# Kernel optimization log

Hardware: AMD Instinct MI355X
Metric: run time of the kernel (lower is better)

The kernel has to match this reference:

```python
import jax, jax.numpy as jnp
import numpy as np
from jax.scipy.special import logsumexp

DEN_SCALE = 1.0  # den_scale from LFMMILoss.__init__


def _log_marginal(em, seqlens, logA, log_start, log_final):
    """Forward (alpha) recursion of a WFSA in log space.
    em: [B,T,S] per-state emission log-likelihoods; logA: [S,S] or [B,S,S].
    Returns per-sequence log-marginal [B].
    """
    B, T, S = em.shape
    alpha0 = log_start + em[:, 0]  # [B,S]

    def step(alpha, xs):
        em_t, t = xs
        # [B,S,1] + [.,S,S] -> logsumexp over source state
        new = logsumexp(alpha[:, :, None] + logA, axis=1) + em_t
        alpha = jnp.where((t < seqlens)[:, None], new, alpha)
        return alpha, None

    em_t_first = jnp.swapaxes(em, 0, 1)  # [T,B,S]
    alpha, _ = jax.lax.scan(step, alpha0, (em_t_first[1:], jnp.arange(1, T)))
    return logsumexp(alpha + log_final, axis=1)  # [B]


def _fsm_logprob(x, seqlens, logA, log_start, log_final, pdf_ids):
    B, T, _ = x.shape
    if pdf_ids.ndim == 1:  # shared graph (denominator)
        em = x[:, :, pdf_ids]  # [B,T,S]
    else:  # per-utterance graphs (numerators), pdf_ids: [B,S]
        S = pdf_ids.shape[-1]
        idx = jnp.broadcast_to(pdf_ids[:, None, :], (B, T, S))
        em = jnp.take_along_axis(x, idx, axis=2)
    return _log_marginal(em, seqlens, logA, log_start, log_final)


def setup_inputs() -> dict:
    key = jax.random.key(0)
    ks = jax.random.split(key, 10)
    B, T, C = 16, 500, 2048
    S_num, S_den = 64, 512
    inp = jax.random.normal(ks[0], (B, T, C), jnp.float32)
    seqlengths = jax.random.randint(ks[1], (B,), T // 2, T + 1, jnp.int32)
    num_logA = jax.nn.log_softmax(jax.random.normal(ks[2], (B, S_num, S_num), jnp.float32), axis=-1)
    num_log_start = jax.nn.log_softmax(jax.random.normal(ks[3], (B, S_num), jnp.float32), axis=-1)
    num_log_final = jax.nn.log_softmax(jax.random.normal(ks[4], (B, S_num), jnp.float32), axis=-1)
    num_pdf_ids = jax.random.randint(ks[5], (B, S_num), 0, C, jnp.int32)
    den_logA = jax.nn.log_softmax(jax.random.normal(ks[6], (S_den, S_den), jnp.float32), axis=-1)
    den_log_start = jax.nn.log_softmax(jax.random.normal(ks[7], (S_den,), jnp.float32), axis=-1)
    den_log_final = jax.nn.log_softmax(jax.random.normal(ks[8], (S_den,), jnp.float32), axis=-1)
    den_pdf_ids = jax.random.randint(ks[9], (S_den,), 0, C, jnp.int32)
    return {
        "input": inp, "seqlengths": seqlengths,
        "num_logA": num_logA, "num_log_start": num_log_start,
        "num_log_final": num_log_final, "num_pdf_ids": num_pdf_ids,
        "den_logA": den_logA, "den_log_start": den_log_start,
        "den_log_final": den_log_final, "den_pdf_ids": den_pdf_ids,
    }


def reference(input, seqlengths, num_logA, num_log_start, num_log_final,
              num_pdf_ids, den_logA, den_log_start, den_log_final, den_pdf_ids):
    x = jnp.clip(input, -30.0, 30.0)
    num_llh = _fsm_logprob(x, seqlengths, num_logA, num_log_start, num_log_final, num_pdf_ids).sum()
    den_llh = _fsm_logprob(x, seqlengths, den_logA, den_log_start, den_log_final, den_pdf_ids).sum()
    return -(num_llh - DEN_SCALE * den_llh)
```

## Files before the change

kernel.cpp:

```cpp
#include <hip/hip_runtime.h>
#include <math.h>

#define BB 16
#define TT 500
#define CC 2048
#define SN 64
#define SD 512
#define NGRP 16
#define NCB 8
#define NDEN 128
#define NTHR 512
#define SHIFTC 30.0f

#define WSF_DACC   32768
#define WSF_DSCALE 32784
#define WSF_NACC   32800
#define WSF_NSCALE 32816

#define AL(p) __hip_atomic_load((p), __ATOMIC_RELAXED, __HIP_MEMORY_SCOPE_AGENT)
#define AS(p, v) __hip_atomic_store((p), (v), __ATOMIC_RELAXED, __HIP_MEMORY_SCOPE_AGENT)

typedef float f4 __attribute__((ext_vector_type(4)));

__device__ __forceinline__ float wave_max(float v) {
  #pragma unroll
  for (int off = 32; off > 0; off >>= 1) v = fmaxf(v, __shfl_xor(v, off, 64));
  return v;
}
__device__ __forceinline__ float wave_sum(float v) {
  #pragma unroll
  for (int off = 32; off > 0; off >>= 1) v += __shfl_xor(v, off, 64);
  return v;
}
__device__ __forceinline__ unsigned long long pk(unsigned tag, float v) {
  return ((unsigned long long)tag << 32) | (unsigned long long)__float_as_uint(v);
}
__device__ __forceinline__ float clamp30(float v) {
  return fminf(fmaxf(v, -30.f), 30.f);
}
__device__ __forceinline__ float rlane(float v, int k) {
  return __uint_as_float(__builtin_amdgcn_readlane(__float_as_uint(v), k));
}

__device__ __forceinline__ void barrier_lds_only() {
  asm volatile("s_waitcnt lgkmcnt(0)" ::: "memory");
  __builtin_amdgcn_s_barrier();
  asm volatile("" ::: "memory");
}

__global__ __launch_bounds__(NTHR, 1) void fsm_fwd(
    const float* __restrict__ x, const int* __restrict__ seqlens,
    const float* __restrict__ nA, const float* __restrict__ nls,
    const float* __restrict__ nlf, const int* __restrict__ npdf,
    const float* __restrict__ dA, const float* __restrict__ dls,
    const float* __restrict__ dlf, const int* __restrict__ dpdf,
    unsigned long long* __restrict__ p64, float* __restrict__ wsf)
{
  __shared__ float prt[2][8 * 64];
  __shared__ float pmx[2][8];
  const int tid = threadIdx.x;
  const int lane = tid & 63, wv = tid >> 6;

  if (blockIdx.x < NDEN) {
    const int g  = blockIdx.x & 15;
    const int cb = blockIdx.x >> 4;
    const int j0 = cb * 64;

    f4 Areg[16];
    {
      const float* Ap = dA + (wv * 64) * SD + j0 + lane;
      #pragma unroll
      for (int k = 0; k < 64; ++k)
        Areg[k >> 2][k & 3] = __expf(Ap[k * SD]);
      #pragma unroll
      for (int r = 0; r < 16; ++r)
        asm volatile("" : "+v"(Areg[r]));
    }

    unsigned long long* gb0 = p64 + (size_t)g * SD;
    unsigned long long* gb1 = p64 + (size_t)(NGRP + g) * SD;

    int pdfj = 0, sl = 0; float lfj = 0.f, pcur = 0.f, scale = SHIFTC;
    float xc = 0.f;
    if (wv == 0) {
      pdfj = dpdf[j0 + lane];
      lfj  = dlf[j0 + lane];
      sl   = seqlens[g];
      float xv = clamp30(x[g * (TT * CC) + pdfj]);
      pcur = __expf(dls[j0 + lane] + xv - SHIFTC);
      AS(gb0 + j0 + lane, pk(0u, pcur));
      xc = clamp30(x[g * (TT * CC) + CC + pdfj]);
    }

    for (int t = 1; t < TT; ++t) {
      unsigned long long* gin  = (t & 1) ? gb0 : gb1;
      unsigned long long* gout = (t & 1) ? gb1 : gb0;

      const unsigned tg = (unsigned)(t - 1);
      unsigned long long* pa = gin + wv * 64 + lane;
      unsigned long long w;
      for (;;) {
        w = AL(pa);
        if ((unsigned)(w >> 32) == tg) break;
        __builtin_amdgcn_s_sleep(1);
      }
      float pv = __uint_as_float((unsigned)w);

      float cm = wave_max(pv);
      if (lane == 0) pmx[t & 1][wv] = cm;

      float q = 0.f;
      #pragma unroll
      for (int k = 0; k < 64; ++k) {
        float pk_ = rlane(pv, k);
        q = fmaf(pk_, Areg[k >> 2][k & 3], q);
      }
      prt[t & 1][wv * 64 + lane] = q;

      barrier_lds_only();

      if (wv == 0) {
        const float* pb = prt[t & 1];
        float qq = 0.f;
        #pragma unroll
        for (int w8 = 0; w8 < 8; ++w8) qq += pb[w8 * 64 + lane];
        float m = pmx[t & 1][0];
        #pragma unroll
        for (int w8 = 1; w8 < 8; ++w8) m = fmaxf(m, pmx[t & 1][w8]);
        float lm = __logf(m);
        if (t < sl) {
          pcur = qq * __expf(xc - SHIFTC - lm);
          scale += SHIFTC + lm;
        }
        AS(gout + j0 + lane, pk((unsigned)t, pcur));
        if (t + 1 < TT)
          xc = clamp30(x[g * (TT * CC) + (t + 1) * CC + pdfj]);
      }
    }
    if (wv == 0) {
      float part = wave_sum(pcur * __expf(lfj));
      if (lane == 0) {
        atomicAdd(wsf + WSF_DACC + g, part);
        if (cb == 0) wsf[WSF_DSCALE + g] = scale;
      }
    }
  } else {
    const int b = blockIdx.x - NDEN;
    if (wv != 0) return;

    f4 Areg[16];
    {
      const float* Ap = nA + b * SN * SN + lane;
      #pragma unroll
      for (int i = 0; i < 64; ++i)
        Areg[i >> 2][i & 3] = __expf(Ap[i * SN]);
      #pragma unroll
      for (int r = 0; r < 16; ++r)
        asm volatile("" : "+v"(Areg[r]));
    }
    const int   pdfj = npdf[b * SN + lane];
    const float lfj  = nlf[b * SN + lane];
    const int   sl   = seqlens[b];
    float xv0 = clamp30(x[b * (TT * CC) + pdfj]);
    float pcur = __expf(nls[b * SN + lane] + xv0 - SHIFTC);
    float scale = SHIFTC;
    float xn = clamp30(x[b * (TT * CC) + CC + pdfj]);

    for (int t = 1; t < TT; ++t) {
      float xv = xn;
      if (t + 1 < TT)
        xn = clamp30(x[b * (TT * CC) + (t + 1) * CC + pdfj]);
      float pold = pcur;
      float q = 0.f;
      #pragma unroll
      for (int i = 0; i < 64; ++i) {
        float pi = rlane(pold, i);
        q = fmaf(pi, Areg[i >> 2][i & 3], q);
      }
      float lm = __logf(wave_max(pold));
      if (t < sl) {
        pcur = q * __expf(xv - SHIFTC - lm);
        scale += SHIFTC + lm;
      }
    }
    float part = wave_sum(pcur * __expf(lfj));
    if (lane == 0) {
      wsf[WSF_NACC + b]   = part;
      wsf[WSF_NSCALE + b] = scale;
    }
  }
}

__global__ void fsm_final(const float* __restrict__ wsf, float* __restrict__ out) {
  const int tid = threadIdx.x;
  float v = 0.f;
  if (tid < 16)
    v = -(wsf[WSF_NSCALE + tid] + __logf(wsf[WSF_NACC + tid]));
  else if (tid < 32)
    v = (wsf[WSF_DSCALE + tid - 16] + __logf(wsf[WSF_DACC + tid - 16]));
  v = wave_sum(v);
  if (tid == 0) out[0] = v;
}

extern "C" void kernel_launch(void* const* d_in, const int* in_sizes, int n_in,
                              void* d_out, int out_size, void* d_ws, size_t ws_size,
                              hipStream_t stream) {
  const float* x    = (const float*)d_in[0];
  const int*   sql  = (const int*)d_in[1];
  const float* nA   = (const float*)d_in[2];
  const float* nls  = (const float*)d_in[3];
  const float* nlf  = (const float*)d_in[4];
  const int*   npdf = (const int*)d_in[5];
  const float* dA   = (const float*)d_in[6];
  const float* dls  = (const float*)d_in[7];
  const float* dlf  = (const float*)d_in[8];
  const int*   dpdf = (const int*)d_in[9];
  float* out = (float*)d_out;
  unsigned long long* p64 = (unsigned long long*)d_ws;
  float* wsf = (float*)d_ws;
  (void)in_sizes; (void)n_in; (void)out_size; (void)ws_size;

  hipMemsetAsync((char*)d_ws + 131072, 0, 256, stream);
  fsm_fwd<<<NDEN + BB, NTHR, 0, stream>>>(x, sql, nA, nls, nlf, npdf,
                                          dA, dls, dlf, dpdf, p64, wsf);
  fsm_final<<<1, 64, 0, stream>>>(wsf, out);
}
```

Baseline: 878.1 us.

## Interleave four denominator sequences per block to hide cross-block sync latency

Each denominator block now advances four batch sequences round-robin instead of one, so it can work on other sequences while the cross-block exchange for one sequence is still in flight. The grid drops from 128 to 32 active denominator blocks, with 32 more launched and exited immediately. The next sequence's state and emission value are prefetched before the barrier. The output update is spread across all eight waves, eight lanes each, instead of only wave 0. The cost is more serial work per block, one LDS barrier per sequence step, and fewer CUs in use.

```diff
diff --git a/kernel.cpp b/kernel.cpp
--- a/kernel.cpp
+++ b/kernel.cpp
@@ -7,8 +7,9 @@
 #define SN 64
 #define SD 512
 #define NGRP 16
-#define NCB 8
-#define NDEN 128
+#define NSETS 4
+#define GPW 4
+#define NDENSLOT 64
 #define NTHR 512
 #define SHIFTC 30.0f
 
@@ -40,6 +41,10 @@
 }
 __device__ __forceinline__ float rlane(float v, int k) {
   return __uint_as_float(__builtin_amdgcn_readlane(__float_as_uint(v), k));
+}
+__device__ __forceinline__ unsigned long long* recbase(
+    unsigned long long* p64, int g, int tag) {
+  return p64 + ((tag & 1) ? (size_t)(NGRP + g) : (size_t)g) * SD;
 }
 
 __device__ __forceinline__ void barrier_lds_only() {
@@ -56,15 +61,17 @@
     const float* __restrict__ dlf, const int* __restrict__ dpdf,
     unsigned long long* __restrict__ p64, float* __restrict__ wsf)
 {
-  __shared__ float prt[2][8 * 64];
+  __shared__ float prt[2][8][64];
   __shared__ float pmx[2][8];
   const int tid = threadIdx.x;
   const int lane = tid & 63, wv = tid >> 6;
 
-  if (blockIdx.x < NDEN) {
-    const int g  = blockIdx.x & 15;
-    const int cb = blockIdx.x >> 4;
+  if (blockIdx.x < NDENSLOT) {
+    if ((blockIdx.x & 7) >= NSETS) return;
+    const int st = blockIdx.x & 7;
+    const int cb = blockIdx.x >> 3;
     const int j0 = cb * 64;
+    const int gbase = st * GPW;
 
     f4 Areg[16];
     {
@@ -77,75 +84,99 @@
         asm volatile("" : "+v"(Areg[r]));
     }
 
-    unsigned long long* gb0 = p64 + (size_t)g * SD;
-    unsigned long long* gb1 = p64 + (size_t)(NGRP + g) * SD;
-
-    int pdfj = 0, sl = 0; float lfj = 0.f, pcur = 0.f, scale = SHIFTC;
-    float xc = 0.f;
-    if (wv == 0) {
-      pdfj = dpdf[j0 + lane];
-      lfj  = dlf[j0 + lane];
-      sl   = seqlens[g];
-      float xv = clamp30(x[g * (TT * CC) + pdfj]);
-      pcur = __expf(dls[j0 + lane] + xv - SHIFTC);
-      AS(gb0 + j0 + lane, pk(0u, pcur));
-      xc = clamp30(x[g * (TT * CC) + CC + pdfj]);
-    }
+    const int oc   = j0 + 8 * wv + (lane & 7);
+    const int pdfo = dpdf[oc];
+    const float lfo = dlf[oc];
+    const float lso = dls[oc];
+
+    int   sl4[GPW];
+    float pc[GPW], sc[GPW];
+    #pragma unroll
+    for (int gk = 0; gk < GPW; ++gk) {
+      const int g = gbase + gk;
+      sl4[gk] = seqlens[g];
+      sc[gk]  = SHIFTC;
+      pc[gk]  = 0.f;
+      if (lane < 8) {
+        float xv = clamp30(x[(size_t)g * (TT * CC) + pdfo]);
+        pc[gk] = __expf(lso + xv - SHIFTC);
+        AS(recbase(p64, g, 0) + oc, pk(0u, pc[gk]));
+      }
+    }
+    unsigned long long pf = AL(recbase(p64, gbase, 0) + wv * 64 + lane);
+    float xn = 0.f;
+    if (lane < 8)
+      xn = clamp30(x[(size_t)gbase * (TT * CC) + CC + pdfo]);
 
     for (int t = 1; t < TT; ++t) {
-      unsigned long long* gin  = (t & 1) ? gb0 : gb1;
-      unsigned long long* gout = (t & 1) ? gb1 : gb0;
-
-      const unsigned tg = (unsigned)(t - 1);
-      unsigned long long* pa = gin + wv * 64 + lane;
-      unsigned long long w;
-      for (;;) {
-        w = AL(pa);
-        if ((unsigned)(w >> 32) == tg) break;
-        __builtin_amdgcn_s_sleep(1);
-      }
-      float pv = __uint_as_float((unsigned)w);
-
-      float cm = wave_max(pv);
-      if (lane == 0) pmx[t & 1][wv] = cm;
-
-      float q = 0.f;
-      #pragma unroll
-      for (int k = 0; k < 64; ++k) {
-        float pk_ = rlane(pv, k);
-        q = fmaf(pk_, Areg[k >> 2][k & 3], q);
-      }
-      prt[t & 1][wv * 64 + lane] = q;
-
-      barrier_lds_only();
-
-      if (wv == 0) {
-        const float* pb = prt[t & 1];
-        float qq = 0.f;
+      #pragma unroll
+      for (int gk = 0; gk < GPW; ++gk) {
+        const int g   = gbase + gk;
+        const int par = gk & 1;
+        const unsigned tg = (unsigned)(t - 1);
+        unsigned long long* pa = recbase(p64, g, t - 1) + wv * 64 + lane;
+
+        unsigned long long w = pf;
+        while ((unsigned)(w >> 32) != tg) {
+          w = AL(pa);
+          if ((unsigned)(w >> 32) == tg) break;
+          __builtin_amdgcn_s_sleep(1);
+        }
+        float pv = __uint_as_float((unsigned)w);
+
+        float cm = wave_max(pv);
+        if (lane == 0) pmx[par][wv] = cm;
+
+        float q = 0.f;
         #pragma unroll
-        for (int w8 = 0; w8 < 8; ++w8) qq += pb[w8 * 64 + lane];
-        float m = pmx[t & 1][0];
-        #pragma unroll
-        for (int w8 = 1; w8 < 8; ++w8) m = fmaxf(m, pmx[t & 1][w8]);
-        float lm = __logf(m);
-        if (t < sl) {
-          pcur = qq * __expf(xc - SHIFTC - lm);
-          scale += SHIFTC + lm;
+        for (int k = 0; k < 64; ++k)
+          q = fmaf(rlane(pv, k), Areg[k >> 2][k & 3], q);
+        prt[par][wv][lane] = q;
+
+        const int  gn = (gk == GPW - 1) ? gbase : g + 1;
+        const int  tn = (gk == GPW - 1) ? t + 1 : t;
+        const bool hn = (tn < TT);
+        float xq = xn;
+        if (hn) {
+          pf = AL(recbase(p64, gn, tn - 1) + wv * 64 + lane);
+          if (lane < 8)
+            xn = clamp30(x[(size_t)gn * (TT * CC) + (size_t)tn * CC + pdfo]);
         }
-        AS(gout + j0 + lane, pk((unsigned)t, pcur));
-        if (t + 1 < TT)
-          xc = clamp30(x[g * (TT * CC) + (t + 1) * CC + pdfj]);
-      }
-    }
-    if (wv == 0) {
-      float part = wave_sum(pcur * __expf(lfj));
-      if (lane == 0) {
+
+        barrier_lds_only();
+
+        if (lane < 8) {
+          float m = pmx[par][0];
+          #pragma unroll
+          for (int w8 = 1; w8 < 8; ++w8) m = fmaxf(m, pmx[par][w8]);
+          float lm = __logf(m);
+          float qq = 0.f;
+          #pragma unroll
+          for (int w8 = 0; w8 < 8; ++w8) qq += prt[par][w8][8 * wv + lane];
+          if (t < sl4[gk]) {
+            pc[gk] = qq * __expf(xq - SHIFTC - lm);
+            sc[gk] += SHIFTC + lm;
+          }
+          AS(recbase(p64, g, t) + oc, pk((unsigned)t, pc[gk]));
+        }
+      }
+    }
+
+    #pragma unroll
+    for (int gk = 0; gk < GPW; ++gk) {
+      const int g = gbase + gk;
+      float v = (lane < 8) ? pc[gk] * __expf(lfo) : 0.f;
+      float part = wave_sum(v);
+      if (lane == 0)
         atomicAdd(wsf + WSF_DACC + g, part);
-        if (cb == 0) wsf[WSF_DSCALE + g] = scale;
-      }
+    }
+    if (cb == 0 && wv == 0 && lane == 0) {
+      #pragma unroll
+      for (int gk = 0; gk < GPW; ++gk)
+        wsf[WSF_DSCALE + gbase + gk] = sc[gk];
     }
   } else {
-    const int b = blockIdx.x - NDEN;
+    const int b = blockIdx.x - NDENSLOT;
     if (wv != 0) return;
 
     f4 Areg[16];
@@ -161,15 +192,15 @@
     const int   pdfj = npdf[b * SN + lane];
     const float lfj  = nlf[b * SN + lane];
     const int   sl   = seqlens[b];
-    float xv0 = clamp30(x[b * (TT * CC) + pdfj]);
+    float xv0 = clamp30(x[(size_t)b * (TT * CC) + pdfj]);
     float pcur = __expf(nls[b * SN + lane] + xv0 - SHIFTC);
     float scale = SHIFTC;
-    float xn = clamp30(x[b * (TT * CC) + CC + pdfj]);
+    float xnn = clamp30(x[(size_t)b * (TT * CC) + CC + pdfj]);
 
     for (int t = 1; t < TT; ++t) {
-      float xv = xn;
+      float xv = xnn;
       if (t + 1 < TT)
-        xn = clamp30(x[b * (TT * CC) + (t + 1) * CC + pdfj]);
+        xnn = clamp30(x[(size_t)b * (TT * CC) + (size_t)(t + 1) * CC + pdfj]);
       float pold = pcur;
       float q = 0.f;
       #pragma unroll
@@ -221,7 +252,7 @@
   (void)in_sizes; (void)n_in; (void)out_size; (void)ws_size;
 
   hipMemsetAsync((char*)d_ws + 131072, 0, 256, stream);
-  fsm_fwd<<<NDEN + BB, NTHR, 0, stream>>>(x, sql, nA, nls, nlf, npdf,
-                                          dA, dls, dlf, dpdf, p64, wsf);
+  fsm_fwd<<<NDENSLOT + BB, NTHR, 0, stream>>>(x, sql, nA, nls, nlf, npdf,
+                                              dA, dls, dlf, dpdf, p64, wsf);
   fsm_final<<<1, 64, 0, stream>>>(wsf, out);
 }
```

New measurement: 2.922 ms. +232.8%, slower.

## Poll cross-block partials with sc0 loads, fall back to atomics, prefetch emissions earlier

Applied to the files above, without the earlier changes.

Cross-block polling of the denominator alpha buffer now first uses sc0-qualified global loads under a small retry budget. If polling keeps failing it falls back to agent-scope atomic loads and eventually disables the fast path. Each producer store is duplicated as an sc0 store plus an atomic store. Emission loads are issued earlier, before the LDS reduction in the denominator path and two steps ahead in the numerator path, to hide global latency. The aim is lower inter-block communication latency per timestep. The cost is extra stores and a reliance on cache-coherence behaviour of sc0 on this hardware.

```diff
diff --git a/kernel.cpp b/kernel.cpp
--- a/kernel.cpp
+++ b/kernel.cpp
@@ -11,6 +11,7 @@
 #define NDEN 128
 #define NTHR 512
 #define SHIFTC 30.0f
+#define SC0_BUDGET 8
 
 #define WSF_DACC   32768
 #define WSF_DSCALE 32784
@@ -21,6 +22,18 @@
 #define AS(p, v) __hip_atomic_store((p), (v), __ATOMIC_RELAXED, __HIP_MEMORY_SCOPE_AGENT)
 
 typedef float f4 __attribute__((ext_vector_type(4)));
+
+__device__ __forceinline__ unsigned long long ld_sc0(const unsigned long long* p) {
+  unsigned long long r;
+  asm volatile("global_load_dwordx2 %0, %1, off sc0\n\t"
+               "s_waitcnt vmcnt(0)"
+               : "=v"(r) : "v"((unsigned long long)p) : "memory");
+  return r;
+}
+__device__ __forceinline__ void st_sc0(unsigned long long* p, unsigned long long v) {
+  asm volatile("global_store_dwordx2 %0, %1, off sc0"
+               :: "v"((unsigned long long)p), "v"(v) : "memory");
+}
 
 __device__ __forceinline__ float wave_max(float v) {
   #pragma unroll
@@ -81,16 +94,21 @@
     unsigned long long* gb1 = p64 + (size_t)(NGRP + g) * SD;
 
     int pdfj = 0, sl = 0; float lfj = 0.f, pcur = 0.f, scale = SHIFTC;
-    float xc = 0.f;
+    float xraw = 0.f;
     if (wv == 0) {
       pdfj = dpdf[j0 + lane];
       lfj  = dlf[j0 + lane];
       sl   = seqlens[g];
       float xv = clamp30(x[g * (TT * CC) + pdfj]);
       pcur = __expf(dls[j0 + lane] + xv - SHIFTC);
-      AS(gb0 + j0 + lane, pk(0u, pcur));
-      xc = clamp30(x[g * (TT * CC) + CC + pdfj]);
-    }
+      unsigned long long rec = pk(0u, pcur);
+      unsigned long long* gp = gb0 + j0 + lane;
+      st_sc0(gp, rec);
+      AS(gp, rec);
+      xraw = x[g * (TT * CC) + CC + pdfj];
+    }
+
+    int budget = SC0_BUDGET, streak = 0;
 
     for (int t = 1; t < TT; ++t) {
       unsigned long long* gin  = (t & 1) ? gb0 : gb1;
@@ -98,13 +116,27 @@
 
       const unsigned tg = (unsigned)(t - 1);
       unsigned long long* pa = gin + wv * 64 + lane;
-      unsigned long long w;
-      for (;;) {
-        w = AL(pa);
-        if ((unsigned)(w >> 32) == tg) break;
+      unsigned long long w = 0;
+      bool ok = false;
+      for (int s = 0; s < budget; ++s) {
+        w = ld_sc0(pa);
+        if ((unsigned)(w >> 32) == tg) { ok = true; break; }
         __builtin_amdgcn_s_sleep(1);
       }
+      const bool allok = __all((int)ok);
+      if (!ok) {
+        for (;;) {
+          w = AL(pa);
+          if ((unsigned)(w >> 32) == tg) break;
+          __builtin_amdgcn_s_sleep(1);
+        }
+      }
+      if (budget) { if (!allok) { if (++streak >= 4) budget = 0; } else streak = 0; }
       float pv = __uint_as_float((unsigned)w);
+
+      float xnew = 0.f;
+      if (wv == 0 && t + 1 < TT)
+        xnew = x[g * (TT * CC) + (t + 1) * CC + pdfj];
 
       float cm = wave_max(pv);
       if (lane == 0) pmx[t & 1][wv] = cm;
@@ -128,13 +160,16 @@
         #pragma unroll
         for (int w8 = 1; w8 < 8; ++w8) m = fmaxf(m, pmx[t & 1][w8]);
         float lm = __logf(m);
+        float xv = clamp30(xraw);
         if (t < sl) {
-          pcur = qq * __expf(xc - SHIFTC - lm);
+          pcur = qq * __expf(xv - SHIFTC - lm);
           scale += SHIFTC + lm;
         }
-        AS(gout + j0 + lane, pk((unsigned)t, pcur));
-        if (t + 1 < TT)
-          xc = clamp30(x[g * (TT * CC) + (t + 1) * CC + pdfj]);
+        unsigned long long rec = pk((unsigned)t, pcur);
+        unsigned long long* gp = gout + j0 + lane;
+        st_sc0(gp, rec);
+        AS(gp, rec);
+        xraw = xnew;
       }
     }
     if (wv == 0) {
@@ -164,12 +199,14 @@
     float xv0 = clamp30(x[b * (TT * CC) + pdfj]);
     float pcur = __expf(nls[b * SN + lane] + xv0 - SHIFTC);
     float scale = SHIFTC;
-    float xn = clamp30(x[b * (TT * CC) + CC + pdfj]);
+    float xr0 = x[b * (TT * CC) + CC + pdfj];
+    float xr1 = (TT > 2) ? x[b * (TT * CC) + 2 * CC + pdfj] : 0.f;
 
     for (int t = 1; t < TT; ++t) {
-      float xv = xn;
-      if (t + 1 < TT)
-        xn = clamp30(x[b * (TT * CC) + (t + 1) * CC + pdfj]);
+      float xv = clamp30(xr0);
+      xr0 = xr1;
+      if (t + 2 < TT)
+        xr1 = x[b * (TT * CC) + (t + 2) * CC + pdfj];
       float pold = pcur;
       float q = 0.f;
       #pragma unroll
```

New measurement: 1.354 ms. +54.2%, slower.

## Spread denominator state finalization across all waves and drop spin-wait sleep

Applied to the files above, without the earlier changes.

The per-step finalization of the 64 owned denominator states moves from wave 0 alone to 8 lanes in each of the 8 waves, so the post-barrier reduction and publish are spread out instead of serialized in one wave. The spin-wait on the global exchange buffer no longer sleeps between polls, aiming to cut wake-up latency on the critical cross-block dependency at the cost of more memory polling traffic. The numerator path prefetches emissions two steps ahead to hide global load latency.

```diff
diff --git a/kernel.cpp b/kernel.cpp
--- a/kernel.cpp
+++ b/kernel.cpp
@@ -7,7 +7,6 @@
 #define SN 64
 #define SD 512
 #define NGRP 16
-#define NCB 8
 #define NDEN 128
 #define NTHR 512
 #define SHIFTC 30.0f
@@ -56,7 +55,7 @@
     const float* __restrict__ dlf, const int* __restrict__ dpdf,
     unsigned long long* __restrict__ p64, float* __restrict__ wsf)
 {
-  __shared__ float prt[2][8 * 64];
+  __shared__ float prt[2][8][64];
   __shared__ float pmx[2][8];
   const int tid = threadIdx.x;
   const int lane = tid & 63, wv = tid >> 6;
@@ -80,21 +79,25 @@
     unsigned long long* gb0 = p64 + (size_t)g * SD;
     unsigned long long* gb1 = p64 + (size_t)(NGRP + g) * SD;
 
-    int pdfj = 0, sl = 0; float lfj = 0.f, pcur = 0.f, scale = SHIFTC;
-    float xc = 0.f;
-    if (wv == 0) {
-      pdfj = dpdf[j0 + lane];
-      lfj  = dlf[j0 + lane];
+    const int  oc   = j0 + 8 * wv + (lane & 7);
+    const bool own  = (lane < 8);
+    int   pdfo = 0, sl = 0;
+    float lfo = 0.f, lso = 0.f, pcur = 0.f, scale = SHIFTC, xraw = 0.f;
+    if (own) {
+      pdfo = dpdf[oc];
+      lfo  = dlf[oc];
+      lso  = dls[oc];
       sl   = seqlens[g];
-      float xv = clamp30(x[g * (TT * CC) + pdfj]);
-      pcur = __expf(dls[j0 + lane] + xv - SHIFTC);
-      AS(gb0 + j0 + lane, pk(0u, pcur));
-      xc = clamp30(x[g * (TT * CC) + CC + pdfj]);
+      float xv = clamp30(x[(size_t)g * (TT * CC) + pdfo]);
+      pcur = __expf(lso + xv - SHIFTC);
+      AS(gb0 + oc, pk(0u, pcur));
+      xraw = x[(size_t)g * (TT * CC) + CC + pdfo];
     }
 
     for (int t = 1; t < TT; ++t) {
       unsigned long long* gin  = (t & 1) ? gb0 : gb1;
       unsigned long long* gout = (t & 1) ? gb1 : gb0;
+      const int par = t & 1;
 
       const unsigned tg = (unsigned)(t - 1);
       unsigned long long* pa = gin + wv * 64 + lane;
@@ -102,12 +105,11 @@
       for (;;) {
         w = AL(pa);
         if ((unsigned)(w >> 32) == tg) break;
-        __builtin_amdgcn_s_sleep(1);
       }
       float pv = __uint_as_float((unsigned)w);
 
       float cm = wave_max(pv);
-      if (lane == 0) pmx[t & 1][wv] = cm;
+      if (lane == 0) pmx[par][wv] = cm;
 
       float q = 0.f;
       #pragma unroll
@@ -115,34 +117,36 @@
         float pk_ = rlane(pv, k);
         q = fmaf(pk_, Areg[k >> 2][k & 3], q);
       }
-      prt[t & 1][wv * 64 + lane] = q;
+      prt[par][wv][lane] = q;
 
       barrier_lds_only();
 
-      if (wv == 0) {
-        const float* pb = prt[t & 1];
+      if (own) {
+        float m = pmx[par][0];
+        #pragma unroll
+        for (int w8 = 1; w8 < 8; ++w8) m = fmaxf(m, pmx[par][w8]);
+        float lm = __logf(m);
         float qq = 0.f;
         #pragma unroll
-        for (int w8 = 0; w8 < 8; ++w8) qq += pb[w8 * 64 + lane];
-        float m = pmx[t & 1][0];
-        #pragma unroll
-        for (int w8 = 1; w8 < 8; ++w8) m = fmaxf(m, pmx[t & 1][w8]);
-        float lm = __logf(m);
+        for (int w8 = 0; w8 < 8; ++w8) qq += prt[par][w8][8 * wv + (lane & 7)];
+        float xv = clamp30(xraw);
         if (t < sl) {
-          pcur = qq * __expf(xc - SHIFTC - lm);
+          pcur = qq * __expf(xv - SHIFTC - lm);
           scale += SHIFTC + lm;
         }
-        AS(gout + j0 + lane, pk((unsigned)t, pcur));
+        AS(gout + oc, pk((unsigned)t, pcur));
         if (t + 1 < TT)
-          xc = clamp30(x[g * (TT * CC) + (t + 1) * CC + pdfj]);
-      }
-    }
-    if (wv == 0) {
-      float part = wave_sum(pcur * __expf(lfj));
-      if (lane == 0) {
+          xraw = x[(size_t)g * (TT * CC) + (size_t)(t + 1) * CC + pdfo];
+      }
+    }
+
+    {
+      float v = own ? pcur * __expf(lfo) : 0.f;
+      float part = wave_sum(v);
+      if (lane == 0)
         atomicAdd(wsf + WSF_DACC + g, part);
-        if (cb == 0) wsf[WSF_DSCALE + g] = scale;
-      }
+      if (cb == 0 && wv == 0 && lane == 0)
+        wsf[WSF_DSCALE + g] = scale;
     }
   } else {
     const int b = blockIdx.x - NDEN;
@@ -161,15 +165,17 @@
     const int   pdfj = npdf[b * SN + lane];
     const float lfj  = nlf[b * SN + lane];
     const int   sl   = seqlens[b];
-    float xv0 = clamp30(x[b * (TT * CC) + pdfj]);
+    float xv0 = clamp30(x[(size_t)b * (TT * CC) + pdfj]);
     float pcur = __expf(nls[b * SN + lane] + xv0 - SHIFTC);
     float scale = SHIFTC;
-    float xn = clamp30(x[b * (TT * CC) + CC + pdfj]);
+    float xr0 = x[(size_t)b * (TT * CC) + CC + pdfj];
+    float xr1 = (TT > 2) ? x[(size_t)b * (TT * CC) + 2 * CC + pdfj] : 0.f;
 
     for (int t = 1; t < TT; ++t) {
-      float xv = xn;
-      if (t + 1 < TT)
-        xn = clamp30(x[b * (TT * CC) + (t + 1) * CC + pdfj]);
+      float xv = clamp30(xr0);
+      xr0 = xr1;
+      if (t + 2 < TT)
+        xr1 = x[(size_t)b * (TT * CC) + (size_t)(t + 2) * CC + pdfj];
       float pold = pcur;
       float q = 0.f;
       #pragma unroll
```

Measured after the change: 1.183 ms. +34.7%, slower.
